# Performance work log

Hardware: AMD Instinct MI355X
Metric: run time of the kernel (lower is better)

## Reference

```python
import jax, jax.numpy as jnp
import numpy as np

B, C, H, W = 4, 32, 544, 960


def setup_inputs() -> dict:
    key = jax.random.key(0)
    k1, k2, k3 = jax.random.split(key, 3)
    tenInput = jax.random.normal(k1, (B, C, H, W), dtype=jnp.float32)
    # flows of a few pixels magnitude, typical for adjacent video frames
    tenFlow = jax.random.normal(k2, (B, 2, H, W), dtype=jnp.float32) * 4.0
    tenMetric = jax.random.normal(k3, (B, 1, H, W), dtype=jnp.float32)
    return {"tenInput": tenInput, "tenFlow": tenFlow, "tenMetric": tenMetric}


def _splat_one(x, flow):
    # x: [C', H, W] values to splat; flow: [2, H, W] (dx, dy)
    Cp, h, w = x.shape
    gy, gx = jnp.meshgrid(jnp.arange(h, dtype=flow.dtype),
                          jnp.arange(w, dtype=flow.dtype), indexing='ij')
    ox = gx + flow[0]  # fractional target x
    oy = gy + flow[1]  # fractional target y
    x0 = jnp.floor(ox)
    y0 = jnp.floor(oy)
    x1 = x0 + 1.0
    y1 = y0 + 1.0
    # bilinear corner weights (NW, NE, SW, SE), identical to CUDA kernel
    w_nw = (x1 - ox) * (y1 - oy)
    w_ne = (ox - x0) * (y1 - oy)
    w_sw = (x1 - ox) * (oy - y0)
    w_se = (ox - x0) * (oy - y0)
    xf = x.reshape(Cp, h * w)
    out = jnp.zeros((Cp, h * w), dtype=x.dtype)
    for cx, cy, wt in ((x0, y0, w_nw), (x1, y0, w_ne), (x0, y1, w_sw), (x1, y1, w_se)):
        ix = cx.astype(jnp.int32)
        iy = cy.astype(jnp.int32)
        valid = (ix >= 0) & (ix < w) & (iy >= 0) & (iy < h)
        wt = jnp.where(valid, wt, 0.0).reshape(h * w)
        idx = (jnp.clip(iy, 0, h - 1) * w + jnp.clip(ix, 0, w - 1)).reshape(h * w)
        out = out.at[:, idx].add(xf * wt[None, :])
    return out.reshape(Cp, h, w)


def softsplat(tenInput, tenFlow, tenMetric, strType):
    if strType == 'average':
        x = jnp.concatenate([tenInput, jnp.ones_like(tenInput[:, :1])], axis=1)
    elif strType == 'linear':
        x = jnp.concatenate([tenInput * tenMetric, tenMetric], axis=1)
    elif strType == 'softmax':
        m = jnp.exp(tenMetric)
        x = jnp.concatenate([tenInput * m, m], axis=1)
    else:  # 'summation'
        x = tenInput
    out = jax.vmap(_splat_one)(x, tenFlow)
    if strType != 'summation':
        norm = out[:, -1:]
        norm = jnp.where(norm == 0.0, 1.0, norm)  # tenNormalize[tenNormalize==0]=1
        out = out[:, :-1] / norm
    return out


def reference(tenInput, tenFlow, tenMetric):
    return softsplat(tenInput, tenFlow, tenMetric, 'softmax')
```

## Files before the change

kernel.cpp:

```cpp
#include <hip/hip_runtime.h>
#include <hip/hip_fp16.h>

constexpr int B = 4, C = 32, H = 544, W = 960;
constexpr int HW = H * W;
constexpr int NPIX = B * HW;

constexpr int TX = 64, TY = 32;
constexpr int PAD = 12;
constexpr int WSX = TX + 2 * PAD;
constexpr int WSY = TY + 2 * PAD;
constexpr int WPIX = WSX * WSY;
constexpr int TILES_X = W / TX;
constexpr int TILES_Y = H / TY;
constexpr int NTILES = TILES_X * TILES_Y;
constexpr int TILE = TX * TY;
constexpr int TPB = 1024;
constexpr int NW = TPB / 64;
constexpr int PPT = TILE / TPB;
constexpr int WIT = (WPIX + TPB - 1) / TPB;
constexpr int CAPE = 9728;
constexpr int MAXFAR = 64;
constexpr int NCH = 4;
constexpr int NPASS = C / NCH;
constexpr int KC = 6;
constexpr unsigned FARCAP = 32768;

struct FarEntry { unsigned key; float a; int p; };

__global__ __launch_bounds__(256)
void far_scan(const float* __restrict__ flow,
              const float* __restrict__ metric,
              unsigned* __restrict__ counter,
              FarEntry* __restrict__ fl)
{
    int idx = blockIdx.x * blockDim.x + threadIdx.x;
    if (idx >= NPIX) return;
    int b = idx / HW;
    int p = idx - b * HW;
    int y = p / W;
    int x = p - y * W;

    float fx = flow[(size_t)(b * 2 + 0) * HW + p];
    float fy = flow[(size_t)(b * 2 + 1) * HW + p];
    if (fabsf(fx) <= (float)(PAD - 2) && fabsf(fy) <= (float)(PAD - 2)) return;

    float ox = (float)x + fx, oy = (float)y + fy;
    float x0f = floorf(ox), y0f = floorf(oy);
    int x0 = (int)x0f, y0 = (int)y0f;
    float wxh = ox - x0f, wxl = 1.0f - wxh;
    float wyh = oy - y0f, wyl = 1.0f - wyh;
    const int   cxs[4] = { x0, x0 + 1, x0,     x0 + 1 };
    const int   cys[4] = { y0, y0,     y0 + 1, y0 + 1 };
    const float wts[4] = { wxl * wyl, wxh * wyl, wxl * wyh, wxh * wyh };
    float m = __expf(metric[(size_t)b * HW + p]);

#pragma unroll
    for (int k = 0; k < 4; ++k) {
        int cx = cxs[k], cy = cys[k];
        if ((unsigned)cx >= (unsigned)W || (unsigned)cy >= (unsigned)H) continue;
        int tx0 = (cx >> 6) << 6;
        int ty0 = (cy >> 5) << 5;
        bool catchable = (x >= tx0 - PAD) && (x < tx0 + TX + PAD) &&
                         (y >= ty0 - PAD) && (y < ty0 + TY + PAD);
        if (!catchable) {
            unsigned slot = atomicAdd(counter, 1u);
            if (slot < FARCAP) {
                int tile = (cy >> 5) * TILES_X + (cx >> 6);
                unsigned lidx = (unsigned)(((cy - ty0) << 6) | (cx - tx0));
                fl[slot] = { ((unsigned)(b * NTILES + tile) << 11) | lidx,
                             wts[k] * m, p };
            }
        }
    }
}

__global__ __launch_bounds__(TPB)
void splat_csr(const float* __restrict__ inp,
               const float* __restrict__ flow,
               const float* __restrict__ metric,
               const unsigned* __restrict__ counter,
               const FarEntry* __restrict__ fl,
               float* __restrict__ out)
{
    __shared__ unsigned entries[CAPE];
    __shared__ __align__(16) unsigned pool[2 * (WPIX + MAXFAR)];
    __shared__ int farPix[MAXFAR];
    __shared__ unsigned wsum[NW];
    __shared__ unsigned farCnt;

    unsigned* offs = pool;
    uint2*    win2 = reinterpret_cast<uint2*>(pool);

    const int t    = threadIdx.x;
    const int tile = blockIdx.x;
    const int b    = blockIdx.y;
    const int tx0  = (tile % TILES_X) * TX;
    const int ty0  = (tile / TILES_X) * TY;
    const unsigned btid = (unsigned)(b * NTILES + tile);

    const float* fxp = flow + (size_t)(b * 2 + 0) * HW;
    const float* fyp = flow + (size_t)(b * 2 + 1) * HW;
    const float* mp  = metric + (size_t)b * HW;

    for (int i = t; i < TILE; i += TPB) offs[i] = 0;
    if (t == 0) farCnt = 0;
    __syncthreads();

    unsigned cr[WIT][4];
#pragma unroll
    for (int j = 0; j < WIT; ++j) {
#pragma unroll
        for (int k = 0; k < 4; ++k) cr[j][k] = 0xFFFF0000u;
        int i = t + j * TPB;
        if (i >= WPIX) continue;
        int wx = i % WSX, wy = i / WSX;
        int gx = tx0 - PAD + wx, gy = ty0 - PAD + wy;
        if ((unsigned)gx >= (unsigned)W || (unsigned)gy >= (unsigned)H) continue;
        int p = gy * W + gx;
        float ox = (float)gx + fxp[p];
        float oy = (float)gy + fyp[p];
        float x0f = floorf(ox), y0f = floorf(oy);
        int lx0 = (int)x0f - tx0, ly0 = (int)y0f - ty0;
        if (lx0 < -1 || lx0 >= TX || ly0 < -1 || ly0 >= TY) continue;
        float wxh = ox - x0f, wxl = 1.0f - wxh;
        float wyh = oy - y0f, wyl = 1.0f - wyh;
        float m = __expf(mp[p]);
        const float w4[4] = { wxl * wyl, wxh * wyl, wxl * wyh, wxh * wyh };
#pragma unroll
        for (int k = 0; k < 4; ++k) {
            int lx = lx0 + (k & 1), ly = ly0 + (k >> 1);
            if ((unsigned)lx < (unsigned)TX && (unsigned)ly < (unsigned)TY) {
                unsigned lidx = (unsigned)((ly << 6) + lx);
                unsigned short ha = __half_as_ushort(__float2half(w4[k] * m));
                cr[j][k] = (lidx << 16) | (unsigned)ha;
                atomicAdd(&offs[lidx], 1u);
            }
        }
    }
    unsigned farN = *counter;
    if (farN > FARCAP) farN = FARCAP;
    for (unsigned e = t; e < farN; e += TPB) {
        unsigned k = fl[e].key;
        if ((k >> 11) == btid) atomicAdd(&offs[k & 2047u], 1u);
    }
    __syncthreads();

    {
        unsigned c0 = offs[2 * t], c1 = offs[2 * t + 1];
        unsigned s = c0 + c1;
        unsigned lane = t & 63, wv = t >> 6;
        unsigned incl = s;
#pragma unroll
        for (int d = 1; d < 64; d <<= 1) {
            unsigned u = __shfl_up(incl, d);
            if (lane >= (unsigned)d) incl += u;
        }
        if (lane == 63) wsum[wv] = incl;
        __syncthreads();
        if (t < 64) {
            unsigned v = (lane < NW) ? wsum[lane] : 0u;
            unsigned inc2 = v;
#pragma unroll
            for (int d = 1; d < 16; d <<= 1) {
                unsigned u = __shfl_up(inc2, d);
                if (lane >= (unsigned)d) inc2 += u;
            }
            if (lane < NW) wsum[lane] = inc2 - v;
        }
        __syncthreads();
        unsigned base = wsum[wv] + (incl - s);
        offs[2 * t]     = base;
        offs[2 * t + 1] = base + c0;
    }
    __syncthreads();

#pragma unroll
    for (int j = 0; j < WIT; ++j) {
#pragma unroll
        for (int k = 0; k < 4; ++k) {
            unsigned c = cr[j][k];
            unsigned lidx = c >> 16;
            if (lidx != 0xFFFFu) {
                unsigned pos = atomicAdd(&offs[lidx], 1u);
                if (pos < CAPE)
                    entries[pos] = ((unsigned)(t + j * TPB) << 16) | (c & 0xFFFFu);
            }
        }
    }
    for (unsigned e = t; e < farN; e += TPB) {
        unsigned k = fl[e].key;
        if ((k >> 11) == btid) {
            unsigned pos = atomicAdd(&offs[k & 2047u], 1u);
            if (pos < CAPE) {
                unsigned idx = atomicAdd(&farCnt, 1u);
                if (idx < MAXFAR) {
                    farPix[idx] = fl[e].p;
                    unsigned short ha = __half_as_ushort(__float2half(fl[e].a));
                    entries[pos] = ((unsigned)(WPIX + idx) << 16) | (unsigned)ha;
                } else {
                    entries[pos] = 0u;
                }
            }
        }
    }
    __syncthreads();

    int qout[PPT];
    unsigned es[PPT], ee[PPT];
    float rn[PPT];
    unsigned ce[PPT][KC];
#pragma unroll
    for (int k = 0; k < PPT; ++k) {
        int sp = t + k * TPB;
        qout[k] = (ty0 + (sp >> 6)) * W + tx0 + (sp & 63);
        unsigned end = min(offs[sp], (unsigned)CAPE);
        unsigned start = min(sp ? offs[sp - 1] : 0u, (unsigned)CAPE);
        if (start > end) start = end;
        es[k] = start; ee[k] = end;
#pragma unroll
        for (int j = 0; j < KC; ++j) {
            unsigned e = start + (unsigned)j;
            ce[k][j] = (e < end) ? entries[e] : 0u;
        }
        float n = 0.0f;
#pragma unroll
        for (int j = 0; j < KC; ++j)
            n += __half2float(__ushort_as_half((unsigned short)(ce[k][j] & 0xFFFFu)));
        for (unsigned e = start + KC; e < end; ++e)
            n += __half2float(__ushort_as_half((unsigned short)(entries[e] & 0xFFFFu)));
        rn[k] = (n == 0.0f) ? 1.0f : 1.0f / n;
    }

    int wp[WIT];
#pragma unroll
    for (int j = 0; j < WIT; ++j) {
        int i = t + j * TPB;
        wp[j] = -1;
        if (i < WPIX) {
            int wx = i % WSX, wy = i / WSX;
            int gx = tx0 - PAD + wx, gy = ty0 - PAD + wy;
            if ((unsigned)gx < (unsigned)W && (unsigned)gy < (unsigned)H)
                wp[j] = gy * W + gx;
        }
    }

    float4 pre[WIT];
    {
        const float* s0 = inp + (size_t)(b * C) * HW;
#pragma unroll
        for (int j = 0; j < WIT; ++j)
            pre[j] = (wp[j] >= 0)
                   ? make_float4(s0[wp[j]], s0[HW + wp[j]],
                                 s0[2 * HW + wp[j]], s0[3 * HW + wp[j]])
                   : make_float4(0.f, 0.f, 0.f, 0.f);
    }
    unsigned nFar = farCnt;
    if (nFar > MAXFAR) nFar = MAXFAR;
    __syncthreads();

    for (int cp = 0; cp < NPASS; ++cp) {
        const float* s0 = inp + (size_t)(b * C + NCH * cp) * HW;

#pragma unroll
        for (int j = 0; j < WIT; ++j) {
            int i = t + j * TPB;
            if (i < WPIX) {
                __half2 h01 = __floats2half2_rn(pre[j].x, pre[j].y);
                __half2 h23 = __floats2half2_rn(pre[j].z, pre[j].w);
                win2[i] = make_uint2(*reinterpret_cast<unsigned*>(&h01),
                                     *reinterpret_cast<unsigned*>(&h23));
            }
        }
        if (t < nFar) {
            int p = farPix[t];
            __half2 h01 = __floats2half2_rn(s0[p], s0[HW + p]);
            __half2 h23 = __floats2half2_rn(s0[2 * HW + p], s0[3 * HW + p]);
            win2[WPIX + t] = make_uint2(*reinterpret_cast<unsigned*>(&h01),
                                        *reinterpret_cast<unsigned*>(&h23));
        }
        __syncthreads();

        if (cp + 1 < NPASS) {
            const float* n0 = inp + (size_t)(b * C + NCH * (cp + 1)) * HW;
#pragma unroll
            for (int j = 0; j < WIT; ++j)
                pre[j] = (wp[j] >= 0)
                       ? make_float4(n0[wp[j]], n0[HW + wp[j]],
                                     n0[2 * HW + wp[j]], n0[3 * HW + wp[j]])
                       : make_float4(0.f, 0.f, 0.f, 0.f);
        }

        float* o0 = out + (size_t)(b * C + NCH * cp) * HW;
#pragma unroll
        for (int k = 0; k < PPT; ++k) {
            __half2 a01 = __floats2half2_rn(0.f, 0.f);
            __half2 a23 = __floats2half2_rn(0.f, 0.f);
#pragma unroll
            for (int j = 0; j < KC; ++j) {
                unsigned ent = ce[k][j];
                uint2 wv = win2[ent >> 16];
                __half2 w2 = __half2half2(__ushort_as_half((unsigned short)(ent & 0xFFFFu)));
                a01 = __hfma2(w2, *reinterpret_cast<__half2*>(&wv.x), a01);
                a23 = __hfma2(w2, *reinterpret_cast<__half2*>(&wv.y), a23);
            }
            for (unsigned e = es[k] + KC; e < ee[k]; ++e) {
                unsigned ent = entries[e];
                uint2 wv = win2[ent >> 16];
                __half2 w2 = __half2half2(__ushort_as_half((unsigned short)(ent & 0xFFFFu)));
                a01 = __hfma2(w2, *reinterpret_cast<__half2*>(&wv.x), a01);
                a23 = __hfma2(w2, *reinterpret_cast<__half2*>(&wv.y), a23);
            }
            int q = qout[k];
            o0[q]          = __low2float(a01)  * rn[k];
            o0[HW + q]     = __high2float(a01) * rn[k];
            o0[2 * HW + q] = __low2float(a23)  * rn[k];
            o0[3 * HW + q] = __high2float(a23) * rn[k];
        }
        __syncthreads();
    }
}


__global__ __launch_bounds__(256)
void splat_f32(const float* __restrict__ inp,
               const float* __restrict__ flow,
               const float* __restrict__ metric,
               float* __restrict__ out,
               float* __restrict__ norm)
{
    int idx = blockIdx.x * blockDim.x + threadIdx.x;
    if (idx >= NPIX) return;
    int b = idx / HW;
    int p = idx - b * HW;
    int y = p / W;
    int x = p - y * W;

    float fx = flow[(b * 2 + 0) * HW + p];
    float fy = flow[(b * 2 + 1) * HW + p];
    float m  = __expf(metric[b * HW + p]);

    float ox = (float)x + fx, oy = (float)y + fy;
    float x0f = floorf(ox), y0f = floorf(oy);
    int x0 = (int)x0f, y0 = (int)y0f;
    float wx1 = ox - x0f, wx0 = 1.0f - wx1;
    float wy1 = oy - y0f, wy0 = 1.0f - wy1;

    float vm[C];
    const float* inb = inp + (size_t)b * C * HW + p;
#pragma unroll
    for (int c = 0; c < C; ++c) vm[c] = inb[(size_t)c * HW] * m;

    float* outb = out + (size_t)b * C * HW;
    float* nrmb = norm + (size_t)b * HW;

    const int   cxs[4] = { x0, x0 + 1, x0,     x0 + 1 };
    const int   cys[4] = { y0, y0,     y0 + 1, y0 + 1 };
    const float wts[4] = { wx0 * wy0, wx1 * wy0, wx0 * wy1, wx1 * wy1 };

#pragma unroll
    for (int k = 0; k < 4; ++k) {
        int cx = cxs[k], cy = cys[k];
        if (cx < 0 || cx >= W || cy < 0 || cy >= H) continue;
        float wt = wts[k];
        int q = cy * W + cx;
        atomicAdd(&nrmb[q], m * wt);
#pragma unroll
        for (int c = 0; c < C; ++c)
            atomicAdd(&outb[(size_t)c * HW + q], vm[c] * wt);
    }
}

__global__ __launch_bounds__(256)
void normalize_f32(float* __restrict__ out, const float* __restrict__ norm)
{
    int t = blockIdx.x * blockDim.x + threadIdx.x;
    long long base = (long long)t * 4;
    if (base >= (long long)B * C * HW) return;
    long long b = base / ((long long)C * HW);
    long long q = base % HW;

    float4 o = *reinterpret_cast<float4*>(out + base);
    float4 n = *reinterpret_cast<const float4*>(norm + b * HW + q);
    o.x /= (n.x == 0.0f ? 1.0f : n.x);
    o.y /= (n.y == 0.0f ? 1.0f : n.y);
    o.z /= (n.z == 0.0f ? 1.0f : n.z);
    o.w /= (n.w == 0.0f ? 1.0f : n.w);
    *reinterpret_cast<float4*>(out + base) = o;
}

extern "C" void kernel_launch(void* const* d_in, const int* in_sizes, int n_in,
                              void* d_out, int out_size, void* d_ws, size_t ws_size,
                              hipStream_t stream) {
    const float* tenInput  = (const float*)d_in[0];
    const float* tenFlow   = (const float*)d_in[1];
    const float* tenMetric = (const float*)d_in[2];
    float* out = (float*)d_out;

    const size_t need = 16 + (size_t)FARCAP * sizeof(FarEntry);

    if (ws_size >= need) {
        unsigned* counter = (unsigned*)d_ws;
        FarEntry* fl = (FarEntry*)((char*)d_ws + 16);

        hipMemsetAsync(counter, 0, 16, stream);
        far_scan<<<(NPIX + 255) / 256, 256, 0, stream>>>(tenFlow, tenMetric, counter, fl);

        dim3 grid(NTILES, B);
        splat_csr<<<grid, TPB, 0, stream>>>(tenInput, tenFlow, tenMetric,
                                            counter, fl, out);
    } else {
        float* norm = (float*)d_ws;
        hipMemsetAsync(out, 0, (size_t)B * C * HW * sizeof(float), stream);
        hipMemsetAsync(norm, 0, (size_t)NPIX * sizeof(float), stream);

        int threads = 256;
        int blocks = (NPIX + threads - 1) / threads;
        splat_f32<<<blocks, threads, 0, stream>>>(tenInput, tenFlow, tenMetric, out, norm);

        long long total = (long long)B * C * HW / 4;
        normalize_f32<<<(int)((total + threads - 1) / threads), threads, 0, stream>>>(out, norm);
    }
}
```

Before: 210.9 us.

## Replace shared-memory CSR gather lists with ELL slots plus global tail

Each output pixel's contributor list moves from a packed CSR array in shared memory to a fixed four-slot ELL entry per pixel, with any extra contributors spilled to a per-tile tail buffer in global workspace. The gather loop reads one uint4 per pixel and runs a fixed four-way unrolled half2 FMA body, removing the variable-length register cache. The cost is a larger workspace requirement, global-memory traffic for the tail entries, and the risk of taking the slow fallback path if the workspace is too small.

```diff
diff --git a/kernel.cpp b/kernel.cpp
--- a/kernel.cpp
+++ b/kernel.cpp
@@ -13,16 +13,17 @@
 constexpr int TILES_X = W / TX;
 constexpr int TILES_Y = H / TY;
 constexpr int NTILES = TILES_X * TILES_Y;
+constexpr int NBT = NTILES * B;
 constexpr int TILE = TX * TY;
 constexpr int TPB = 1024;
 constexpr int NW = TPB / 64;
 constexpr int PPT = TILE / TPB;
 constexpr int WIT = (WPIX + TPB - 1) / TPB;
-constexpr int CAPE = 9728;
+constexpr int KELL = 4;
 constexpr int MAXFAR = 64;
+constexpr int TAILCAP = 4096;
 constexpr int NCH = 4;
 constexpr int NPASS = C / NCH;
-constexpr int KC = 6;
 constexpr unsigned FARCAP = 32768;
 
 struct FarEntry { unsigned key; float a; int p; };
@@ -75,21 +76,23 @@
 }
 
 __global__ __launch_bounds__(TPB)
-void splat_csr(const float* __restrict__ inp,
+void splat_ell(const float* __restrict__ inp,
                const float* __restrict__ flow,
                const float* __restrict__ metric,
                const unsigned* __restrict__ counter,
                const FarEntry* __restrict__ fl,
+               unsigned* __restrict__ tailG,
                float* __restrict__ out)
 {
-    __shared__ unsigned entries[CAPE];
-    __shared__ __align__(16) unsigned pool[2 * (WPIX + MAXFAR)];
+    __shared__ __align__(16) uint4 ell4[TILE];
+    __shared__ unsigned short tailStart[TILE];
     __shared__ int farPix[MAXFAR];
+    __shared__ __align__(16) uint2 pool2[WPIX + MAXFAR];
     __shared__ unsigned wsum[NW];
-    __shared__ unsigned farCnt;
-
-    unsigned* offs = pool;
-    uint2*    win2 = reinterpret_cast<uint2*>(pool);
+    __shared__ unsigned farCnt, tailTot;
+
+    unsigned* cnt  = reinterpret_cast<unsigned*>(pool2);
+    uint2*    win2 = pool2;
 
     const int t    = threadIdx.x;
     const int tile = blockIdx.x;
@@ -97,13 +100,17 @@
     const int tx0  = (tile % TILES_X) * TX;
     const int ty0  = (tile / TILES_X) * TY;
     const unsigned btid = (unsigned)(b * NTILES + tile);
+    unsigned* tailT = tailG + (size_t)btid * TAILCAP;
 
     const float* fxp = flow + (size_t)(b * 2 + 0) * HW;
     const float* fyp = flow + (size_t)(b * 2 + 1) * HW;
     const float* mp  = metric + (size_t)b * HW;
 
-    for (int i = t; i < TILE; i += TPB) offs[i] = 0;
-    if (t == 0) farCnt = 0;
+    for (int i = t; i < TILE; i += TPB) {
+        cnt[i] = 0;
+        ell4[i] = make_uint4(0u, 0u, 0u, 0u);
+    }
+    if (t == 0) { farCnt = 0; }
     __syncthreads();
 
     unsigned cr[WIT][4];
@@ -133,7 +140,7 @@
                 unsigned lidx = (unsigned)((ly << 6) + lx);
                 unsigned short ha = __half_as_ushort(__float2half(w4[k] * m));
                 cr[j][k] = (lidx << 16) | (unsigned)ha;
-                atomicAdd(&offs[lidx], 1u);
+                atomicAdd(&cnt[lidx], 1u);
             }
         }
     }
@@ -141,13 +148,15 @@
     if (farN > FARCAP) farN = FARCAP;
     for (unsigned e = t; e < farN; e += TPB) {
         unsigned k = fl[e].key;
-        if ((k >> 11) == btid) atomicAdd(&offs[k & 2047u], 1u);
+        if ((k >> 11) == btid) atomicAdd(&cnt[k & 2047u], 1u);
     }
     __syncthreads();
 
     {
-        unsigned c0 = offs[2 * t], c1 = offs[2 * t + 1];
-        unsigned s = c0 + c1;
+        unsigned c0 = cnt[2 * t], c1 = cnt[2 * t + 1];
+        unsigned e0 = c0 > KELL ? c0 - KELL : 0u;
+        unsigned e1 = c1 > KELL ? c1 - KELL : 0u;
+        unsigned s = e0 + e1;
         unsigned lane = t & 63, wv = t >> 6;
         unsigned incl = s;
 #pragma unroll
@@ -169,8 +178,11 @@
         }
         __syncthreads();
         unsigned base = wsum[wv] + (incl - s);
-        offs[2 * t]     = base;
-        offs[2 * t + 1] = base + c0;
+        tailStart[2 * t]     = (unsigned short)base;
+        tailStart[2 * t + 1] = (unsigned short)(base + e0);
+        if (t == TPB - 1) tailTot = base + s;
+        cnt[2 * t] = 0;
+        cnt[2 * t + 1] = 0;
     }
     __syncthreads();
 
@@ -181,53 +193,62 @@
             unsigned c = cr[j][k];
             unsigned lidx = c >> 16;
             if (lidx != 0xFFFFu) {
-                unsigned pos = atomicAdd(&offs[lidx], 1u);
-                if (pos < CAPE)
-                    entries[pos] = ((unsigned)(t + j * TPB) << 16) | (c & 0xFFFFu);
+                unsigned word = ((unsigned)(t + j * TPB) << 16) | (c & 0xFFFFu);
+                unsigned r = atomicAdd(&cnt[lidx], 1u);
+                if (r < KELL) {
+                    reinterpret_cast<unsigned*>(ell4)[4 * lidx + r] = word;
+                } else {
+                    unsigned pos = (unsigned)tailStart[lidx] + (r - KELL);
+                    if (pos < TAILCAP) tailT[pos] = word;
+                }
             }
         }
     }
     for (unsigned e = t; e < farN; e += TPB) {
         unsigned k = fl[e].key;
         if ((k >> 11) == btid) {
-            unsigned pos = atomicAdd(&offs[k & 2047u], 1u);
-            if (pos < CAPE) {
-                unsigned idx = atomicAdd(&farCnt, 1u);
-                if (idx < MAXFAR) {
-                    farPix[idx] = fl[e].p;
-                    unsigned short ha = __half_as_ushort(__float2half(fl[e].a));
-                    entries[pos] = ((unsigned)(WPIX + idx) << 16) | (unsigned)ha;
-                } else {
-                    entries[pos] = 0u;
-                }
-            }
-        }
-    }
+            unsigned lidx = k & 2047u;
+            unsigned idx = atomicAdd(&farCnt, 1u);
+            unsigned word;
+            if (idx < MAXFAR) {
+                farPix[idx] = fl[e].p;
+                unsigned short ha = __half_as_ushort(__float2half(fl[e].a));
+                word = ((unsigned)(WPIX + idx) << 16) | (unsigned)ha;
+            } else {
+                word = 0u;
+            }
+            unsigned r = atomicAdd(&cnt[lidx], 1u);
+            if (r < KELL) {
+                reinterpret_cast<unsigned*>(ell4)[4 * lidx + r] = word;
+            } else {
+                unsigned pos = (unsigned)tailStart[lidx] + (r - KELL);
+                if (pos < TAILCAP) tailT[pos] = word;
+            }
+        }
+    }
+    __threadfence_block();
     __syncthreads();
 
     int qout[PPT];
-    unsigned es[PPT], ee[PPT];
+    unsigned ts_[PPT], te_[PPT];
     float rn[PPT];
-    unsigned ce[PPT][KC];
+    unsigned tTot = tailTot;
 #pragma unroll
     for (int k = 0; k < PPT; ++k) {
         int sp = t + k * TPB;
         qout[k] = (ty0 + (sp >> 6)) * W + tx0 + (sp & 63);
-        unsigned end = min(offs[sp], (unsigned)CAPE);
-        unsigned start = min(sp ? offs[sp - 1] : 0u, (unsigned)CAPE);
-        if (start > end) start = end;
-        es[k] = start; ee[k] = end;
-#pragma unroll
-        for (int j = 0; j < KC; ++j) {
-            unsigned e = start + (unsigned)j;
-            ce[k][j] = (e < end) ? entries[e] : 0u;
-        }
-        float n = 0.0f;
-#pragma unroll
-        for (int j = 0; j < KC; ++j)
-            n += __half2float(__ushort_as_half((unsigned short)(ce[k][j] & 0xFFFFu)));
-        for (unsigned e = start + KC; e < end; ++e)
-            n += __half2float(__ushort_as_half((unsigned short)(entries[e] & 0xFFFFu)));
+        uint4 e4 = ell4[sp];
+        float n = __half2float(__ushort_as_half((unsigned short)(e4.x & 0xFFFFu)))
+                + __half2float(__ushort_as_half((unsigned short)(e4.y & 0xFFFFu)))
+                + __half2float(__ushort_as_half((unsigned short)(e4.z & 0xFFFFu)))
+                + __half2float(__ushort_as_half((unsigned short)(e4.w & 0xFFFFu)));
+        unsigned ts = tailStart[sp];
+        unsigned te = (sp < TILE - 1) ? (unsigned)tailStart[sp + 1] : tTot;
+        if (te > TAILCAP) te = TAILCAP;
+        if (ts > te) ts = te;
+        ts_[k] = ts; te_[k] = te;
+        for (unsigned e = ts; e < te; ++e)
+            n += __half2float(__ushort_as_half((unsigned short)(tailT[e] & 0xFFFFu)));
         rn[k] = (n == 0.0f) ? 1.0f : 1.0f / n;
     }
 
@@ -243,7 +264,6 @@
                 wp[j] = gy * W + gx;
         }
     }
-
     float4 pre[WIT];
     {
         const float* s0 = inp + (size_t)(b * C) * HW;
@@ -271,7 +291,7 @@
                                      *reinterpret_cast<unsigned*>(&h23));
             }
         }
-        if (t < nFar) {
+        if (t < (int)nFar) {
             int p = farPix[t];
             __half2 h01 = __floats2half2_rn(s0[p], s0[HW + p]);
             __half2 h23 = __floats2half2_rn(s0[2 * HW + p], s0[3 * HW + p]);
@@ -293,18 +313,30 @@
         float* o0 = out + (size_t)(b * C + NCH * cp) * HW;
 #pragma unroll
         for (int k = 0; k < PPT; ++k) {
+            int sp = t + k * TPB;
+            uint4 e4 = ell4[sp];
             __half2 a01 = __floats2half2_rn(0.f, 0.f);
             __half2 a23 = __floats2half2_rn(0.f, 0.f);
-#pragma unroll
-            for (int j = 0; j < KC; ++j) {
-                unsigned ent = ce[k][j];
-                uint2 wv = win2[ent >> 16];
-                __half2 w2 = __half2half2(__ushort_as_half((unsigned short)(ent & 0xFFFFu)));
-                a01 = __hfma2(w2, *reinterpret_cast<__half2*>(&wv.x), a01);
-                a23 = __hfma2(w2, *reinterpret_cast<__half2*>(&wv.y), a23);
-            }
-            for (unsigned e = es[k] + KC; e < ee[k]; ++e) {
-                unsigned ent = entries[e];
+            {
+                uint2 wv0 = win2[e4.x >> 16];
+                uint2 wv1 = win2[e4.y >> 16];
+                uint2 wv2 = win2[e4.z >> 16];
+                uint2 wv3 = win2[e4.w >> 16];
+                __half2 w0 = __half2half2(__ushort_as_half((unsigned short)(e4.x & 0xFFFFu)));
+                __half2 w1 = __half2half2(__ushort_as_half((unsigned short)(e4.y & 0xFFFFu)));
+                __half2 w2 = __half2half2(__ushort_as_half((unsigned short)(e4.z & 0xFFFFu)));
+                __half2 w3 = __half2half2(__ushort_as_half((unsigned short)(e4.w & 0xFFFFu)));
+                a01 = __hfma2(w0, *reinterpret_cast<__half2*>(&wv0.x), a01);
+                a23 = __hfma2(w0, *reinterpret_cast<__half2*>(&wv0.y), a23);
+                a01 = __hfma2(w1, *reinterpret_cast<__half2*>(&wv1.x), a01);
+                a23 = __hfma2(w1, *reinterpret_cast<__half2*>(&wv1.y), a23);
+                a01 = __hfma2(w2, *reinterpret_cast<__half2*>(&wv2.x), a01);
+                a23 = __hfma2(w2, *reinterpret_cast<__half2*>(&wv2.y), a23);
+                a01 = __hfma2(w3, *reinterpret_cast<__half2*>(&wv3.x), a01);
+                a23 = __hfma2(w3, *reinterpret_cast<__half2*>(&wv3.y), a23);
+            }
+            for (unsigned e = ts_[k]; e < te_[k]; ++e) {
+                unsigned ent = tailT[e];
                 uint2 wv = win2[ent >> 16];
                 __half2 w2 = __half2half2(__ushort_as_half((unsigned short)(ent & 0xFFFFu)));
                 a01 = __hfma2(w2, *reinterpret_cast<__half2*>(&wv.x), a01);
@@ -396,18 +428,24 @@
     const float* tenMetric = (const float*)d_in[2];
     float* out = (float*)d_out;
 
-    const size_t need = 16 + (size_t)FARCAP * sizeof(FarEntry);
-
-    if (ws_size >= need) {
-        unsigned* counter = (unsigned*)d_ws;
-        FarEntry* fl = (FarEntry*)((char*)d_ws + 16);
+    size_t off = 0;
+    auto alloc = [&](size_t bytes) { size_t o = off; off += (bytes + 15) & ~(size_t)15; return o; };
+    size_t oCnt  = alloc(16);
+    size_t oFl   = alloc((size_t)FARCAP * sizeof(FarEntry));
+    size_t oTail = alloc((size_t)NBT * TAILCAP * 4);
+
+    if (ws_size >= off) {
+        char* ws = (char*)d_ws;
+        unsigned* counter = (unsigned*)(ws + oCnt);
+        FarEntry* fl      = (FarEntry*)(ws + oFl);
+        unsigned* tailG   = (unsigned*)(ws + oTail);
 
         hipMemsetAsync(counter, 0, 16, stream);
         far_scan<<<(NPIX + 255) / 256, 256, 0, stream>>>(tenFlow, tenMetric, counter, fl);
 
         dim3 grid(NTILES, B);
-        splat_csr<<<grid, TPB, 0, stream>>>(tenInput, tenFlow, tenMetric,
-                                            counter, fl, out);
+        splat_ell<<<grid, TPB, 0, stream>>>(tenInput, tenFlow, tenMetric,
+                                            counter, fl, tailG, out);
     } else {
         float* norm = (float*)d_ws;
         hipMemsetAsync(out, 0, (size_t)B * C * HW * sizeof(float), stream);
```

New measurement: 228.3 us. +8.2%, slower.
